# Optimization experiments

Hardware: AMD Instinct MI355X
Metric: run time of the kernel (lower is better)

The kernel has to match this reference:

```python
import jax, jax.numpy as jnp
import numpy as np

N_NODES = 100000
IN_CH = 256
OUT_CH = 128
HEADS = 1
N_EDGES = 1600000
NEG_SLOPE = 0.2
EPS = 1e-16


def setup_inputs() -> dict:
    key = jax.random.key(0)
    ks = jax.random.split(key, 6)
    x = jax.random.normal(ks[0], (N_NODES, IN_CH), dtype=jnp.float32)
    edge_index = jax.random.randint(ks[1], (2, N_EDGES), 0, N_NODES, dtype=jnp.int64)
    # xavier-ish scaled params
    lin_src = jax.random.normal(ks[2], (IN_CH, OUT_CH), dtype=jnp.float32) * (1.414 * (2.0 / (IN_CH + OUT_CH)) ** 0.5)
    att_src = jax.random.normal(ks[3], (1, HEADS, OUT_CH), dtype=jnp.float32) * 0.1
    att_dst = jax.random.normal(ks[4], (1, HEADS, OUT_CH), dtype=jnp.float32) * 0.1
    bias = jnp.zeros((HEADS * OUT_CH,), dtype=jnp.float32)
    return {"x": x, "edge_index": edge_index, "lin_src": lin_src,
            "att_src": att_src, "att_dst": att_dst, "bias": bias}


def reference(x, edge_index, lin_src, att_src, att_dst, bias):
    N = x.shape[0]
    # shared projection (lin_dst is lin_src when in_channels is an int)
    xp = (x @ lin_src).reshape(N, HEADS, OUT_CH)  # [N, H, C]

    # add_self_loops: drop existing self-edges (via mask) and append N loop edges
    src, dst = edge_index[0], edge_index[1]
    loop = jnp.arange(N, dtype=edge_index.dtype)
    src_all = jnp.concatenate([src, loop])
    dst_all = jnp.concatenate([dst, loop])
    valid = jnp.concatenate([src != dst, jnp.ones((N,), dtype=bool)])  # [E+N]

    # per-node attention logits
    alpha_src = jnp.sum(xp * att_src, axis=-1)  # [N, H]
    alpha_dst = jnp.sum(xp * att_dst, axis=-1)  # [N, H]
    alpha = alpha_src[src_all] + alpha_dst[dst_all]  # [E+N, H]
    alpha = jax.nn.leaky_relu(alpha, NEG_SLOPE)

    # scatter softmax over incoming edges of each dst node (global-max stabilized,
    # matching the original src.max() over all retained edges)
    amax = jnp.max(jnp.where(valid[:, None], alpha, -jnp.inf))
    ex = jnp.exp(alpha - amax) * valid[:, None].astype(alpha.dtype)
    denom = jax.ops.segment_sum(ex, dst_all, num_segments=N)  # [N, H]
    alpha = ex / (denom[dst_all] + EPS)  # [E+N, H]

    # weighted aggregation
    weighted = xp[src_all] * alpha[..., None]  # [E+N, H, C]
    out = jax.ops.segment_sum(weighted, dst_all, num_segments=N)  # [N, H, C]

    out = out.reshape(N, HEADS * OUT_CH) + bias  # concat=True
    return out
```

## Files before the change

kernel.cpp:

```cpp
#include <hip/hip_runtime.h>
#include <cstdint>
#include <cstddef>

#define IN_CH 256
#define OUT_CH 128
#define NEG_SLOPE 0.2f
#define EPS 1e-16f

typedef __attribute__((ext_vector_type(8))) short bf16x8;
typedef __attribute__((ext_vector_type(4))) float f32x4;

__device__ __forceinline__ unsigned short f2bf(float f) {
    unsigned int u = __float_as_uint(f);
    return (unsigned short)((u + 0x7fffu + ((u >> 16) & 1u)) >> 16);
}

__global__ __launch_bounds__(256) void convert_w_kernel(const float* __restrict__ w,
                                                        unsigned short* __restrict__ wt)
{
    const int n = blockIdx.x;
    const int k = threadIdx.x;
    wt[(size_t)n * IN_CH + k] = f2bf(w[(size_t)k * OUT_CH + n]);
}

__global__ __launch_bounds__(256) void convert_x_kernel(
    const float* __restrict__ x, unsigned short* __restrict__ xb, long long nquad)
{
    const long long stride = (long long)gridDim.x * blockDim.x;
    for (long long i = (long long)blockIdx.x * blockDim.x + threadIdx.x;
         i < nquad; i += stride) {
        float4 v = ((const float4*)x)[i];
        ushort4 o;
        o.x = f2bf(v.x); o.y = f2bf(v.y); o.z = f2bf(v.z); o.w = f2bf(v.w);
        ((ushort4*)xb)[i] = o;
    }
}

__global__ __launch_bounds__(256) void gemm_kernel(
    const unsigned short* __restrict__ xb, const unsigned short* __restrict__ wt,
    const float* __restrict__ att_s, const float* __restrict__ att_d,
    unsigned short* __restrict__ xpb, float* __restrict__ asrc, float* __restrict__ adst,
    int M)
{
    const int bid  = blockIdx.x;
    const int tid  = threadIdx.x;
    const int wv   = tid >> 6;
    const int lane = tid & 63;
    const int lm   = lane & 15;
    const int quad = lane >> 4;
    const int arow = bid * 64 + wv * 16 + lm;
    const bool av  = arow < M;
    const unsigned short* xrow = xb + (size_t)arow * IN_CH + quad * 8;

    f32x4 acc[8];
#pragma unroll
    for (int t = 0; t < 8; ++t) acc[t] = (f32x4){0.f, 0.f, 0.f, 0.f};

#pragma unroll
    for (int kk = 0; kk < 8; ++kk) {
        const int k0 = kk * 32;
        bf16x8 af = {0, 0, 0, 0, 0, 0, 0, 0};
        if (av) af = *(const bf16x8*)(xrow + k0);
#pragma unroll
        for (int t = 0; t < 8; ++t) {
            bf16x8 bf = *(const bf16x8*)(wt + (size_t)(16 * t + lm) * IN_CH + k0 + quad * 8);
            acc[t] = __builtin_amdgcn_mfma_f32_16x16x32_bf16(af, bf, acc[t], 0, 0, 0);
        }
    }

    float asw[8], adw[8];
#pragma unroll
    for (int t = 0; t < 8; ++t) {
        asw[t] = att_s[16 * t + lm];
        adw[t] = att_d[16 * t + lm];
    }
#pragma unroll
    for (int r = 0; r < 4; ++r) {
        const int orow = bid * 64 + wv * 16 + quad * 4 + r;
        if (orow < M) {
            float ps = 0.f, pd = 0.f;
            unsigned short* xr = xpb + (size_t)orow * OUT_CH + lm;
#pragma unroll
            for (int t = 0; t < 8; ++t) {
                float v = acc[t][r];
                xr[16 * t] = f2bf(v);
                ps += v * asw[t];
                pd += v * adw[t];
            }
#pragma unroll
            for (int m = 1; m < 16; m <<= 1) {
                ps += __shfl_xor(ps, m, 16);
                pd += __shfl_xor(pd, m, 16);
            }
            if (lm == 0) { asrc[orow] = ps; adst[orow] = pd; }
        }
    }
}

__global__ __launch_bounds__(256) void hist_kernel(
    const int* __restrict__ src, const int* __restrict__ dst,
    int* __restrict__ deg, int* __restrict__ pw, int E, int nblk)
{
    const int T = nblk * 256;
    const int e0 = blockIdx.x * 256 + threadIdx.x;
#pragma unroll
    for (int k = 0; k < 8; ++k) {
        const int e = e0 + k * T;
        if (e < E) {
            int s = src[e], d = dst[e];
            if (s != d) pw[e] = atomicAdd(&deg[d], 1);
        }
    }
}

#define SCAN_NB 256
#define SCAN_NT 256

__global__ __launch_bounds__(SCAN_NT) void scan_partial_kernel(
    const int* __restrict__ deg, int* __restrict__ bsum, int N)
{
    __shared__ int sh[SCAN_NT];
    const int chunk = (N + SCAN_NB - 1) / SCAN_NB;
    const int sub   = (chunk + SCAN_NT - 1) / SCAN_NT;
    const int b0 = blockIdx.x * chunk;
    const int t0 = b0 + threadIdx.x * sub;
    const int t1 = min(min(b0 + chunk, t0 + sub), N);
    int s = 0;
    for (int i = t0; i < t1; ++i) s += deg[i];
    sh[threadIdx.x] = s;
    __syncthreads();
    for (int off = SCAN_NT / 2; off > 0; off >>= 1) {
        if (threadIdx.x < off) sh[threadIdx.x] += sh[threadIdx.x + off];
        __syncthreads();
    }
    if (threadIdx.x == 0) bsum[blockIdx.x] = sh[0];
}

__global__ __launch_bounds__(SCAN_NB) void scan_blocksums_kernel(
    const int* __restrict__ bsum, int* __restrict__ boff,
    int* __restrict__ row_ptr, int N)
{
    __shared__ int sh[SCAN_NB];
    const int t = threadIdx.x;
    sh[t] = bsum[t];
    __syncthreads();
    for (int off = 1; off < SCAN_NB; off <<= 1) {
        int v = (t >= off) ? sh[t - off] : 0;
        __syncthreads();
        sh[t] += v;
        __syncthreads();
    }
    boff[t] = (t == 0) ? 0 : sh[t - 1];
    if (t == SCAN_NB - 1) row_ptr[N] = sh[t];
}

__global__ __launch_bounds__(SCAN_NT) void scan_fill_kernel(
    const int* __restrict__ deg, const int* __restrict__ boff,
    int* __restrict__ row_ptr, int N)
{
    __shared__ int sh[SCAN_NT];
    const int chunk = (N + SCAN_NB - 1) / SCAN_NB;
    const int sub   = (chunk + SCAN_NT - 1) / SCAN_NT;
    const int b0 = blockIdx.x * chunk;
    const int t0 = b0 + threadIdx.x * sub;
    const int t1 = min(min(b0 + chunk, t0 + sub), N);
    int s = 0;
    for (int i = t0; i < t1; ++i) s += deg[i];
    sh[threadIdx.x] = s;
    __syncthreads();
    for (int off = 1; off < SCAN_NT; off <<= 1) {
        int v = (threadIdx.x >= off) ? sh[threadIdx.x - off] : 0;
        __syncthreads();
        sh[threadIdx.x] += v;
        __syncthreads();
    }
    int run = boff[blockIdx.x] + ((threadIdx.x == 0) ? 0 : sh[threadIdx.x - 1]);
    for (int i = t0; i < t1; ++i) {
        row_ptr[i] = run;
        run += deg[i];
    }
}

__global__ __launch_bounds__(256) void scatter_kernel(
    const int* __restrict__ src, const int* __restrict__ dst,
    const int* __restrict__ row_ptr, const int* __restrict__ pw,
    int* __restrict__ col, int E, int nblk)
{
    const int T = nblk * 256;
    const int e0 = blockIdx.x * 256 + threadIdx.x;
#pragma unroll
    for (int k = 0; k < 8; ++k) {
        const int e = e0 + k * T;
        if (e < E) {
            int s = src[e], d = dst[e];
            if (s != d) col[row_ptr[d] + pw[e]] = s;
        }
    }
}

__global__ __launch_bounds__(256) void aggregate_kernel(
    const unsigned short* __restrict__ xpb, const float* __restrict__ asrc,
    const float* __restrict__ adst, const int* __restrict__ row_ptr,
    const int* __restrict__ col, const float* __restrict__ bias,
    float* __restrict__ out, int N)
{
    const int n = (int)((blockIdx.x * blockDim.x + threadIdx.x) >> 6);
    const int lane = threadIdx.x & 63;
    if (n >= N) return;
    const float a_d = adst[n];
    const unsigned int* xpw = (const unsigned int*)xpb;

    float ax0 = 0.f, ay0 = 0.f, ax1 = 0.f, ay1 = 0.f;
    float ax2 = 0.f, ay2 = 0.f, ax3 = 0.f, ay3 = 0.f;
    float den = 0.f;

    {
        float lg = asrc[n] + a_d;
        lg = (lg > 0.f) ? lg : lg * NEG_SLOPE;
        float ex = __expf(lg);
        den += ex;
        unsigned int v = xpw[(size_t)n * 64 + lane];
        ax0 += ex * __uint_as_float(v << 16);
        ay0 += ex * __uint_as_float(v & 0xffff0000u);
    }

    const int beg = row_ptr[n], end = row_ptr[n + 1];
    for (int base = beg; base < end; base += 64) {
        const int idx = base + lane;
        int s = 0; float ex = 0.f;
        if (idx < end) {
            s = col[idx];
            float lg = asrc[s] + a_d;
            lg = (lg > 0.f) ? lg : lg * NEG_SLOPE;
            ex = __expf(lg);
        }
        const int cnt = min(64, end - base);
        int j = 0;
        for (; j + 4 <= cnt; j += 4) {
            float e0 = __shfl(ex, j, 64),     e1 = __shfl(ex, j + 1, 64);
            float e2 = __shfl(ex, j + 2, 64), e3 = __shfl(ex, j + 3, 64);
            int   s0 = __shfl(s, j, 64),      s1 = __shfl(s, j + 1, 64);
            int   s2 = __shfl(s, j + 2, 64),  s3 = __shfl(s, j + 3, 64);
            unsigned int v0 = xpw[(size_t)s0 * 64 + lane];
            unsigned int v1 = xpw[(size_t)s1 * 64 + lane];
            unsigned int v2 = xpw[(size_t)s2 * 64 + lane];
            unsigned int v3 = xpw[(size_t)s3 * 64 + lane];
            den += (e0 + e1) + (e2 + e3);
            ax0 += e0 * __uint_as_float(v0 << 16);
            ay0 += e0 * __uint_as_float(v0 & 0xffff0000u);
            ax1 += e1 * __uint_as_float(v1 << 16);
            ay1 += e1 * __uint_as_float(v1 & 0xffff0000u);
            ax2 += e2 * __uint_as_float(v2 << 16);
            ay2 += e2 * __uint_as_float(v2 & 0xffff0000u);
            ax3 += e3 * __uint_as_float(v3 << 16);
            ay3 += e3 * __uint_as_float(v3 & 0xffff0000u);
        }
        for (; j < cnt; ++j) {
            float e0 = __shfl(ex, j, 64);
            int   s0 = __shfl(s, j, 64);
            unsigned int v0 = xpw[(size_t)s0 * 64 + lane];
            den += e0;
            ax0 += e0 * __uint_as_float(v0 << 16);
            ay0 += e0 * __uint_as_float(v0 & 0xffff0000u);
        }
    }

    const float inv = 1.f / (den + EPS);
    const float2 bv = ((const float2*)bias)[lane];
    float2 o;
    o.x = ((ax0 + ax1) + (ax2 + ax3)) * inv + bv.x;
    o.y = ((ay0 + ay1) + (ay2 + ay3)) * inv + bv.y;
    ((float2*)out)[(size_t)n * 64 + lane] = o;
}

extern "C" void kernel_launch(void* const* d_in, const int* in_sizes, int n_in,
                              void* d_out, int out_size, void* d_ws, size_t ws_size,
                              hipStream_t stream)
{
    const float* x     = (const float*)d_in[0];
    const int*   ei    = (const int*)d_in[1];
    const float* w     = (const float*)d_in[2];
    const float* att_s = (const float*)d_in[3];
    const float* att_d = (const float*)d_in[4];
    const float* bias  = (const float*)d_in[5];
    float* out = (float*)d_out;

    const int N = in_sizes[0] / IN_CH;
    const int E = in_sizes[1] / 2;
    const int* src = ei;
    const int* dst = ei + E;

    char* p = (char*)d_ws;
    auto take = [&](size_t bytes) { char* q = p; p += (bytes + 255) & ~size_t(255); return q; };
    unsigned short* xpb = (unsigned short*)take((size_t)N * OUT_CH * 2);
    unsigned short* wt  = (unsigned short*)take((size_t)OUT_CH * IN_CH * 2);
    unsigned short* xb  = (unsigned short*)take((size_t)N * IN_CH * 2);
    float* asrc   = (float*)take((size_t)N * 4);
    float* adst   = (float*)take((size_t)N * 4);
    int*   deg    = (int*)take((size_t)N * 4);
    int*   row_ptr= (int*)take((size_t)(N + 1) * 4);
    int*   bsum   = (int*)take(SCAN_NB * 4);
    int*   boff   = (int*)take(SCAN_NB * 4);
    int*   pw     = (int*)take((size_t)E * 4);
    int*   col    = (int*)take((size_t)E * 4);

    hipMemsetAsync(deg, 0, (size_t)N * 4, stream);
    convert_w_kernel<<<OUT_CH, IN_CH, 0, stream>>>(w, wt);

    const long long nquad = (long long)N * IN_CH / 4;
    convert_x_kernel<<<2048, 256, 0, stream>>>(x, xb, nquad);

    const int hist_blocks = (E + 256 * 8 - 1) / (256 * 8);
    hist_kernel<<<hist_blocks, 256, 0, stream>>>(src, dst, deg, pw, E, hist_blocks);

    const int gemm_blocks = (N + 63) / 64;
    gemm_kernel<<<gemm_blocks, 256, 0, stream>>>(xb, wt, att_s, att_d, xpb, asrc, adst, N);

    scan_partial_kernel<<<SCAN_NB, SCAN_NT, 0, stream>>>(deg, bsum, N);
    scan_blocksums_kernel<<<1, SCAN_NB, 0, stream>>>(bsum, boff, row_ptr, N);
    scan_fill_kernel<<<SCAN_NB, SCAN_NT, 0, stream>>>(deg, boff, row_ptr, N);

    const int sc_blocks = (E + 256 * 8 - 1) / (256 * 8);
    scatter_kernel<<<sc_blocks, 256, 0, stream>>>(src, dst, row_ptr, pw, col, E, sc_blocks);

    aggregate_kernel<<<(N + 3) / 4, 256, 0, stream>>>(
        xpb, asrc, adst, row_ptr, col, bias, out, N);
}
```

Before: 414.0 us.

## Merge independent preprocessing kernels into block-partitioned launches and unroll aggregation by eight

Measured after the change: 384.0 us. 7.3% less time.

```diff
diff --git a/kernel.cpp b/kernel.cpp
--- a/kernel.cpp
+++ b/kernel.cpp
@@ -15,20 +15,28 @@
     return (unsigned short)((u + 0x7fffu + ((u >> 16) & 1u)) >> 16);
 }
 
-__global__ __launch_bounds__(256) void convert_w_kernel(const float* __restrict__ w,
-                                                        unsigned short* __restrict__ wt)
-{
-    const int n = blockIdx.x;
-    const int k = threadIdx.x;
-    wt[(size_t)n * IN_CH + k] = f2bf(w[(size_t)k * OUT_CH + n]);
-}
-
-__global__ __launch_bounds__(256) void convert_x_kernel(
-    const float* __restrict__ x, unsigned short* __restrict__ xb, long long nquad)
-{
-    const long long stride = (long long)gridDim.x * blockDim.x;
-    for (long long i = (long long)blockIdx.x * blockDim.x + threadIdx.x;
-         i < nquad; i += stride) {
+__device__ __forceinline__ void hist_body(
+    int bid, int nblk, const int* __restrict__ src, const int* __restrict__ dst,
+    int* __restrict__ deg, int* __restrict__ pw, int E)
+{
+    const int T = nblk * 256;
+    const int e0 = bid * 256 + threadIdx.x;
+#pragma unroll
+    for (int k = 0; k < 8; ++k) {
+        const int e = e0 + k * T;
+        if (e < E) {
+            int s = src[e], d = dst[e];
+            if (s != d) pw[e] = atomicAdd(&deg[d], 1);
+        }
+    }
+}
+
+__device__ __forceinline__ void convert_x_body(
+    int bid, int nblk, const float* __restrict__ x, unsigned short* __restrict__ xb,
+    long long nquad)
+{
+    const long long stride = (long long)nblk * 256;
+    for (long long i = (long long)bid * 256 + threadIdx.x; i < nquad; i += stride) {
         float4 v = ((const float4*)x)[i];
         ushort4 o;
         o.x = f2bf(v.x); o.y = f2bf(v.y); o.z = f2bf(v.z); o.w = f2bf(v.w);
@@ -36,13 +44,54 @@
     }
 }
 
-__global__ __launch_bounds__(256) void gemm_kernel(
-    const unsigned short* __restrict__ xb, const unsigned short* __restrict__ wt,
+__global__ __launch_bounds__(256) void fused_pre_kernel(
+    const int* __restrict__ src, const int* __restrict__ dst,
+    int* __restrict__ deg, int* __restrict__ pw, int E, int hist_blocks,
+    const float* __restrict__ x, unsigned short* __restrict__ xb, long long nquad,
+    int cx_blocks,
+    const float* __restrict__ w, unsigned short* __restrict__ wt)
+{
+    const int b = blockIdx.x;
+    if (b < hist_blocks) {
+        hist_body(b, hist_blocks, src, dst, deg, pw, E);
+    } else if (b < hist_blocks + cx_blocks) {
+        convert_x_body(b - hist_blocks, cx_blocks, x, xb, nquad);
+    } else {
+        const int n = b - hist_blocks - cx_blocks;
+        const int k = threadIdx.x;
+        wt[(size_t)n * IN_CH + k] = f2bf(w[(size_t)k * OUT_CH + n]);
+    }
+}
+
+#define SCAN_NB 256
+#define SCAN_NT 256
+
+__device__ __forceinline__ void scan_partial_body(
+    int bid, const int* __restrict__ deg, int* __restrict__ bsum, int N)
+{
+    __shared__ int sh[SCAN_NT];
+    const int chunk = (N + SCAN_NB - 1) / SCAN_NB;
+    const int sub   = (chunk + SCAN_NT - 1) / SCAN_NT;
+    const int b0 = bid * chunk;
+    const int t0 = b0 + threadIdx.x * sub;
+    const int t1 = min(min(b0 + chunk, t0 + sub), N);
+    int s = 0;
+    for (int i = t0; i < t1; ++i) s += deg[i];
+    sh[threadIdx.x] = s;
+    __syncthreads();
+    for (int off = SCAN_NT / 2; off > 0; off >>= 1) {
+        if (threadIdx.x < off) sh[threadIdx.x] += sh[threadIdx.x + off];
+        __syncthreads();
+    }
+    if (threadIdx.x == 0) bsum[bid] = sh[0];
+}
+
+__device__ __forceinline__ void gemm_body(
+    int bid, const unsigned short* __restrict__ xb, const unsigned short* __restrict__ wt,
     const float* __restrict__ att_s, const float* __restrict__ att_d,
     unsigned short* __restrict__ xpb, float* __restrict__ asrc, float* __restrict__ adst,
     int M)
 {
-    const int bid  = blockIdx.x;
     const int tid  = threadIdx.x;
     const int wv   = tid >> 6;
     const int lane = tid & 63;
@@ -97,43 +146,16 @@
     }
 }
 
-__global__ __launch_bounds__(256) void hist_kernel(
-    const int* __restrict__ src, const int* __restrict__ dst,
-    int* __restrict__ deg, int* __restrict__ pw, int E, int nblk)
-{
-    const int T = nblk * 256;
-    const int e0 = blockIdx.x * 256 + threadIdx.x;
-#pragma unroll
-    for (int k = 0; k < 8; ++k) {
-        const int e = e0 + k * T;
-        if (e < E) {
-            int s = src[e], d = dst[e];
-            if (s != d) pw[e] = atomicAdd(&deg[d], 1);
-        }
-    }
-}
-
-#define SCAN_NB 256
-#define SCAN_NT 256
-
-__global__ __launch_bounds__(SCAN_NT) void scan_partial_kernel(
-    const int* __restrict__ deg, int* __restrict__ bsum, int N)
-{
-    __shared__ int sh[SCAN_NT];
-    const int chunk = (N + SCAN_NB - 1) / SCAN_NB;
-    const int sub   = (chunk + SCAN_NT - 1) / SCAN_NT;
-    const int b0 = blockIdx.x * chunk;
-    const int t0 = b0 + threadIdx.x * sub;
-    const int t1 = min(min(b0 + chunk, t0 + sub), N);
-    int s = 0;
-    for (int i = t0; i < t1; ++i) s += deg[i];
-    sh[threadIdx.x] = s;
-    __syncthreads();
-    for (int off = SCAN_NT / 2; off > 0; off >>= 1) {
-        if (threadIdx.x < off) sh[threadIdx.x] += sh[threadIdx.x + off];
-        __syncthreads();
-    }
-    if (threadIdx.x == 0) bsum[blockIdx.x] = sh[0];
+__global__ __launch_bounds__(256) void fused_gemm_scan_kernel(
+    const unsigned short* __restrict__ xb, const unsigned short* __restrict__ wt,
+    const float* __restrict__ att_s, const float* __restrict__ att_d,
+    unsigned short* __restrict__ xpb, float* __restrict__ asrc, float* __restrict__ adst,
+    int M, const int* __restrict__ deg, int* __restrict__ bsum)
+{
+    if ((int)blockIdx.x < SCAN_NB)
+        scan_partial_body(blockIdx.x, deg, bsum, M);
+    else
+        gemm_body(blockIdx.x - SCAN_NB, xb, wt, att_s, att_d, xpb, asrc, adst, M);
 }
 
 __global__ __launch_bounds__(SCAN_NB) void scan_blocksums_kernel(
@@ -236,6 +258,41 @@
         }
         const int cnt = min(64, end - base);
         int j = 0;
+        for (; j + 8 <= cnt; j += 8) {
+            float e0 = __shfl(ex, j, 64),     e1 = __shfl(ex, j + 1, 64);
+            float e2 = __shfl(ex, j + 2, 64), e3 = __shfl(ex, j + 3, 64);
+            float e4 = __shfl(ex, j + 4, 64), e5 = __shfl(ex, j + 5, 64);
+            float e6 = __shfl(ex, j + 6, 64), e7 = __shfl(ex, j + 7, 64);
+            int   s0 = __shfl(s, j, 64),      s1 = __shfl(s, j + 1, 64);
+            int   s2 = __shfl(s, j + 2, 64),  s3 = __shfl(s, j + 3, 64);
+            int   s4 = __shfl(s, j + 4, 64),  s5 = __shfl(s, j + 5, 64);
+            int   s6 = __shfl(s, j + 6, 64),  s7 = __shfl(s, j + 7, 64);
+            unsigned int v0 = xpw[(size_t)s0 * 64 + lane];
+            unsigned int v1 = xpw[(size_t)s1 * 64 + lane];
+            unsigned int v2 = xpw[(size_t)s2 * 64 + lane];
+            unsigned int v3 = xpw[(size_t)s3 * 64 + lane];
+            unsigned int v4 = xpw[(size_t)s4 * 64 + lane];
+            unsigned int v5 = xpw[(size_t)s5 * 64 + lane];
+            unsigned int v6 = xpw[(size_t)s6 * 64 + lane];
+            unsigned int v7 = xpw[(size_t)s7 * 64 + lane];
+            den += ((e0 + e1) + (e2 + e3)) + ((e4 + e5) + (e6 + e7));
+            ax0 += e0 * __uint_as_float(v0 << 16);
+            ay0 += e0 * __uint_as_float(v0 & 0xffff0000u);
+            ax1 += e1 * __uint_as_float(v1 << 16);
+            ay1 += e1 * __uint_as_float(v1 & 0xffff0000u);
+            ax2 += e2 * __uint_as_float(v2 << 16);
+            ay2 += e2 * __uint_as_float(v2 & 0xffff0000u);
+            ax3 += e3 * __uint_as_float(v3 << 16);
+            ay3 += e3 * __uint_as_float(v3 & 0xffff0000u);
+            ax0 += e4 * __uint_as_float(v4 << 16);
+            ay0 += e4 * __uint_as_float(v4 & 0xffff0000u);
+            ax1 += e5 * __uint_as_float(v5 << 16);
+            ay1 += e5 * __uint_as_float(v5 & 0xffff0000u);
+            ax2 += e6 * __uint_as_float(v6 << 16);
+            ay2 += e6 * __uint_as_float(v6 & 0xffff0000u);
+            ax3 += e7 * __uint_as_float(v7 << 16);
+            ay3 += e7 * __uint_as_float(v7 & 0xffff0000u);
+        }
         for (; j + 4 <= cnt; j += 4) {
             float e0 = __shfl(ex, j, 64),     e1 = __shfl(ex, j + 1, 64);
             float e2 = __shfl(ex, j + 2, 64), e3 = __shfl(ex, j + 3, 64);
@@ -305,18 +362,18 @@
     int*   col    = (int*)take((size_t)E * 4);
 
     hipMemsetAsync(deg, 0, (size_t)N * 4, stream);
-    convert_w_kernel<<<OUT_CH, IN_CH, 0, stream>>>(w, wt);
-
+
+    const int hist_blocks = (E + 256 * 8 - 1) / (256 * 8);
+    const int cx_blocks = 1024;
     const long long nquad = (long long)N * IN_CH / 4;
-    convert_x_kernel<<<2048, 256, 0, stream>>>(x, xb, nquad);
-
-    const int hist_blocks = (E + 256 * 8 - 1) / (256 * 8);
-    hist_kernel<<<hist_blocks, 256, 0, stream>>>(src, dst, deg, pw, E, hist_blocks);
+    fused_pre_kernel<<<hist_blocks + cx_blocks + OUT_CH, 256, 0, stream>>>(
+        src, dst, deg, pw, E, hist_blocks,
+        x, xb, nquad, cx_blocks, w, wt);
 
     const int gemm_blocks = (N + 63) / 64;
-    gemm_kernel<<<gemm_blocks, 256, 0, stream>>>(xb, wt, att_s, att_d, xpb, asrc, adst, N);
-
-    scan_partial_kernel<<<SCAN_NB, SCAN_NT, 0, stream>>>(deg, bsum, N);
+    fused_gemm_scan_kernel<<<SCAN_NB + gemm_blocks, 256, 0, stream>>>(
+        xb, wt, att_s, att_d, xpb, asrc, adst, N, deg, bsum);
+
     scan_blocksums_kernel<<<1, SCAN_NB, 0, stream>>>(bsum, boff, row_ptr, N);
     scan_fill_kernel<<<SCAN_NB, SCAN_NT, 0, stream>>>(deg, boff, row_ptr, N);
 
```
